# Kernel tuning notes

Hardware: AMD Instinct MI355X
Metric: run time of the kernel (lower is better)

Reference implementation:

```python
import jax, jax.numpy as jnp
import numpy as np

B = 32
NEG_INF = -1e30


def _conv2d(x, w, b):
    # x: (B,C,H,W), w: (O,I,kh,kw), VALID, stride 1
    y = jax.lax.conv_general_dilated(x, w, (1, 1), 'VALID',
                                     dimension_numbers=('NCHW', 'OIHW', 'NCHW'))
    return y + b[None, :, None, None]


def _maxpool_3_2_1(x):
    return jax.lax.reduce_window(x, NEG_INF, jax.lax.max,
                                 (1, 1, 3, 3), (1, 1, 2, 2),
                                 ((0, 0), (0, 0), (1, 1), (1, 1)))


def _extract_patches(x, kh, kw, stride):
    # x: (B,C,H,W) -> (B,C,oh,kh,ow,kw)
    H, W = x.shape[2], x.shape[3]
    oh = (H - kh) // stride + 1
    ow = (W - kw) // stride + 1
    rows = jnp.arange(oh)[:, None] * stride + jnp.arange(kh)[None, :]  # (oh,kh)
    cols = jnp.arange(ow)[:, None] * stride + jnp.arange(kw)[None, :]  # (ow,kw)
    return x[:, :, rows][:, :, :, :, cols]  # (B,C,oh,kh,ow,kw)


def _local_conv(x, w, b, stride):
    # unshared-weight conv. w: (oh,ow,oc,ic,kh,kw), b: (oc,oh,ow)
    kh, kw = w.shape[4], w.shape[5]
    p = _extract_patches(x, kh, kw, stride)              # (B,ic,oh,kh,ow,kw)
    y = jnp.einsum('bcpkql,pqockl->bopq', p, w)          # (B,oc,oh,ow)
    return y + b[None]


def setup_inputs() -> dict:
    key = jax.random.key(0)
    ks = jax.random.split(key, 14)
    s = 0.05
    f32 = jnp.float32
    inp = {
        'x': jax.random.normal(ks[0], (B, 3, 152, 152), dtype=f32),
        'conv1_w': jax.random.normal(ks[1], (32, 3, 11, 11), dtype=f32) * s,
        'conv1_b': jax.random.normal(ks[2], (32,), dtype=f32) * s,
        'conv2_w': jax.random.normal(ks[3], (16, 32, 9, 9), dtype=f32) * s,
        'conv2_b': jax.random.normal(ks[4], (16,), dtype=f32) * s,
        'lc1_w': jax.random.normal(ks[5], (55, 55, 16, 16, 9, 9), dtype=f32) * s,
        'lc1_b': jax.random.normal(ks[6], (16, 55, 55), dtype=f32) * s,
        'lc2_w': jax.random.normal(ks[7], (25, 25, 16, 16, 7, 7), dtype=f32) * s,
        'lc2_b': jax.random.normal(ks[8], (16, 25, 25), dtype=f32) * s,
        'lc3_w': jax.random.normal(ks[9], (21, 21, 16, 16, 5, 5), dtype=f32) * s,
        'lc3_b': jax.random.normal(ks[10], (16, 21, 21), dtype=f32) * s,
        'fc1_w': jax.random.normal(ks[11], (4096, 16 * 21 * 21), dtype=f32) * s,
        'fc1_b': jax.random.normal(ks[12], (4096,), dtype=f32) * s,
    }
    return inp


def reference(x, conv1_w, conv1_b, conv2_w, conv2_b,
              lc1_w, lc1_b, lc2_w, lc2_b, lc3_w, lc3_b,
              fc1_w, fc1_b):
    h = jax.nn.relu(_conv2d(x, conv1_w, conv1_b))        # (B,32,142,142)
    h = _maxpool_3_2_1(h)                                # (B,32,71,71)
    h = jax.nn.relu(_conv2d(h, conv2_w, conv2_b))        # (B,16,63,63)
    h = jax.nn.relu(_local_conv(h, lc1_w, lc1_b, 1))     # (B,16,55,55)
    h = jax.nn.relu(_local_conv(h, lc2_w, lc2_b, 2))     # (B,16,25,25)
    h = jax.nn.relu(_local_conv(h, lc3_w, lc3_b, 1))     # (B,16,21,21)
    h = h.reshape(h.shape[0], 16 * 21 * 21)
    return h @ fc1_w.T + fc1_b                           # (B,4096)
```

## Files before the change

kernel.cpp:

```cpp
#include <hip/hip_runtime.h>
#include <cstddef>

typedef __attribute__((ext_vector_type(8))) short bf16x8;
typedef __attribute__((ext_vector_type(8), aligned(8))) short bf16x8a;
typedef __attribute__((ext_vector_type(4))) float f32x4;
typedef __attribute__((ext_vector_type(4))) unsigned short u16x4;
typedef __attribute__((ext_vector_type(8))) unsigned short u16x8;

__device__ inline unsigned short f2bf(float f) {
  unsigned int u = __float_as_uint(f);
  unsigned int r = (u + 0x7FFFu + ((u >> 16) & 1u)) >> 16;
  return (unsigned short)r;
}
__device__ inline float bf2f(unsigned short u) {
  return __uint_as_float((unsigned int)u << 16);
}

__global__ __launch_bounds__(256) void prep_xb1(const float* __restrict__ x,
                                                unsigned short* __restrict__ xb) {
  const int j = blockIdx.x * 256 + threadIdx.x;
  const int iw = j % 160;
  const int ih = (j / 160) % 152;
  const int b = j / (160 * 152);
  unsigned short v[4] = {0, 0, 0, 0};
  if (iw < 152) {
    #pragma unroll
    for (int ic = 0; ic < 3; ++ic)
      v[ic] = f2bf(x[(size_t)(b * 3 + ic) * 23104 + ih * 152 + iw]);
  }
  *(unsigned long long*)(xb + ((((size_t)ih * 160 + iw) * 32) + b) * 4) =
      *(unsigned long long*)v;
}

__global__ __launch_bounds__(256) void prep_wb1(const float* __restrict__ w,
                                                unsigned short* __restrict__ wb) {
  const int j = blockIdx.x * 256 + threadIdx.x;
  const int e = j & 7;
  const int s = (j >> 3) & 31;
  const int kcj = j >> 8;
  const int kc = kcj & 3, step = kcj >> 2;
  const int t = step * 8 + kc * 2 + (e >> 2);
  const int ics = e & 3;
  const int kh = t / 12, kwp = t - kh * 12;
  float val = 0.f;
  if (t < 132 && kwp < 11 && ics < 3)
    val = w[((s * 3 + ics) * 11 + kh) * 11 + kwp];
  wb[j] = f2bf(val);
}

__global__ __launch_bounds__(256, 4) void conv1_mfma(const unsigned short* __restrict__ xb,
                                                     const unsigned short* __restrict__ wb,
                                                     const float* __restrict__ bias,
                                                     unsigned short* __restrict__ outB) {
  const int lane = threadIdx.x & 63;
  const int wvi = threadIdx.x >> 6;
  const int pos = blockIdx.x * 4 + wvi;
  const int oh = pos / 142, ow = pos % 142;
  const int row = lane & 15;
  const int kc = lane >> 4;
  f32x4 a00 = {0.f, 0.f, 0.f, 0.f}, a01 = a00, a10 = a00, a11 = a00;

  #pragma unroll 2
  for (int j = 0; j < 17; ++j) {
    const int t0 = j * 8 + 2 * kc;
    int kh = t0 / 12;
    int kwp = t0 - kh * 12;
    if (t0 >= 132) { kh = 0; kwp = 0; }
    const bf16x8 wa0 = *(const bf16x8*)(wb + (((j * 4 + kc) * 32) + row) * 8);
    const bf16x8 wa1 = *(const bf16x8*)(wb + (((j * 4 + kc) * 32) + 16 + row) * 8);
    const size_t base = (((size_t)(oh + kh) * 160) + (ow + kwp)) * 128;
    const unsigned short* xp0 = xb + base + row * 4;
    bf16x8 xv0, xv1;
    ((unsigned long long*)&xv0)[0] = *(const unsigned long long*)(xp0);
    ((unsigned long long*)&xv0)[1] = *(const unsigned long long*)(xp0 + 128);
    ((unsigned long long*)&xv1)[0] = *(const unsigned long long*)(xp0 + 64);
    ((unsigned long long*)&xv1)[1] = *(const unsigned long long*)(xp0 + 192);
    a00 = __builtin_amdgcn_mfma_f32_16x16x32_bf16(wa0, xv0, a00, 0, 0, 0);
    a01 = __builtin_amdgcn_mfma_f32_16x16x32_bf16(wa0, xv1, a01, 0, 0, 0);
    a10 = __builtin_amdgcn_mfma_f32_16x16x32_bf16(wa1, xv0, a10, 0, 0, 0);
    a11 = __builtin_amdgcn_mfma_f32_16x16x32_bf16(wa1, xv1, a11, 0, 0, 0);
  }

  unsigned short* ob = outB + (size_t)pos * 1024;
  u16x4 p00, p01, p10, p11;
  #pragma unroll
  for (int r = 0; r < 4; ++r) {
    const float bv0 = bias[kc * 4 + r];
    const float bv1 = bias[16 + kc * 4 + r];
    p00[r] = f2bf(fmaxf(a00[r] + bv0, 0.f));
    p01[r] = f2bf(fmaxf(a01[r] + bv0, 0.f));
    p10[r] = f2bf(fmaxf(a10[r] + bv1, 0.f));
    p11[r] = f2bf(fmaxf(a11[r] + bv1, 0.f));
  }
  *(u16x4*)(ob + row * 32 + kc * 4) = p00;
  *(u16x4*)(ob + (row + 16) * 32 + kc * 4) = p01;
  *(u16x4*)(ob + row * 32 + 16 + kc * 4) = p10;
  *(u16x4*)(ob + (row + 16) * 32 + 16 + kc * 4) = p11;
}

__global__ __launch_bounds__(256) void pool_t2(const unsigned short* __restrict__ in,
                                               unsigned short* __restrict__ xb) {
  const int tid = threadIdx.x;
  const int b = tid & 31, pg = tid >> 5;
  const int posp = blockIdx.x * 8 + pg;
  if (posp >= 5041) return;
  const int ohp = posp / 71, owp = posp % 71;
  u16x8 m[4];
  #pragma unroll
  for (int q = 0; q < 4; ++q)
    #pragma unroll
    for (int e = 0; e < 8; ++e) m[q][e] = 0;

  #pragma unroll
  for (int kh = 0; kh < 3; ++kh) {
    const int ih = ohp * 2 - 1 + kh;
    if (ih < 0 || ih >= 142) continue;
    #pragma unroll
    for (int kw = 0; kw < 3; ++kw) {
      const int iw = owp * 2 - 1 + kw;
      if (iw < 0 || iw >= 142) continue;
      const u16x8* p =
          (const u16x8*)(in + (((size_t)(ih * 142 + iw)) * 32 + b) * 32);
      #pragma unroll
      for (int q = 0; q < 4; ++q) {
        const u16x8 v = p[q];
        #pragma unroll
        for (int e = 0; e < 8; ++e) m[q][e] = (v[e] > m[q][e]) ? v[e] : m[q][e];
      }
    }
  }
  u16x8* o = (u16x8*)(xb + ((size_t)posp * 32 + b) * 32);
  #pragma unroll
  for (int q = 0; q < 4; ++q) o[q] = m[q];
}

__global__ __launch_bounds__(256) void prep_wb2(const float* __restrict__ w,
                                                unsigned short* __restrict__ wb) {
  const int j = blockIdx.x * 256 + threadIdx.x;
  if (j >= 81 * 16 * 32) return;
  const int ic = j & 31, oc = (j >> 5) & 15, sp = j >> 9;
  wb[j] = f2bf(w[(size_t)oc * 2592 + ic * 81 + sp]);
}

__global__ __launch_bounds__(256) void conv2_mfma(const unsigned short* __restrict__ xb,
                                                  const unsigned short* __restrict__ wb,
                                                  const float* __restrict__ bias,
                                                  unsigned short* __restrict__ outB) {
  const int lane = threadIdx.x & 63;
  const int wvi = threadIdx.x >> 6;
  int pos = blockIdx.x * 4 + wvi;
  if (pos > 3968) pos = 3968;
  const int oh = pos / 63, ow = pos % 63;
  const int row = lane & 15;
  const int kc = lane >> 4;
  f32x4 acc0 = {0.f, 0.f, 0.f, 0.f}, acc1 = {0.f, 0.f, 0.f, 0.f};
  const unsigned short* xbase = xb + (size_t)(oh * 71 + ow) * 1024;
  const int aoff = row * 32 + kc * 8;
  const int boff0 = aoff;
  const int boff1 = (row + 16) * 32 + kc * 8;

  #pragma unroll
  for (int kh = 0; kh < 9; ++kh) {
    #pragma unroll
    for (int kw = 0; kw < 9; ++kw) {
      const int sp = kh * 9 + kw;
      const bf16x8 a = *(const bf16x8*)(wb + sp * 512 + aoff);
      const unsigned short* xp = xbase + (kh * 71 + kw) * 1024;
      const bf16x8 b0 = *(const bf16x8*)(xp + boff0);
      const bf16x8 b1 = *(const bf16x8*)(xp + boff1);
      acc0 = __builtin_amdgcn_mfma_f32_16x16x32_bf16(a, b0, acc0, 0, 0, 0);
      acc1 = __builtin_amdgcn_mfma_f32_16x16x32_bf16(a, b1, acc1, 0, 0, 0);
    }
  }

  u16x4 pk0, pk1;
  #pragma unroll
  for (int r = 0; r < 4; ++r) {
    const float bv = bias[kc * 4 + r];
    pk0[r] = f2bf(fmaxf(acc0[r] + bv, 0.f));
    pk1[r] = f2bf(fmaxf(acc1[r] + bv, 0.f));
  }
  *(u16x4*)(outB + (size_t)pos * 512 + row * 16 + kc * 4) = pk0;
  *(u16x4*)(outB + (size_t)pos * 512 + (row + 16) * 16 + kc * 4) = pk1;
}

template <int KH>
__global__ __launch_bounds__(256) void prep_lcw(const float* __restrict__ w,
                                                unsigned short* __restrict__ wbT,
                                                int pos_base) {
  constexpr int KHW = KH * KH;
  constexpr int P = (KHW + 1) / 2;
  __shared__ float ls[8 * 16 * KHW];
  const int tid = threadIdx.x;
  const float* wp = w + (size_t)(pos_base + blockIdx.x) * (256 * KHW);
  unsigned short* ob = wbT + (size_t)blockIdx.x * (P * 512);

  for (int half = 0; half < 2; ++half) {
    __syncthreads();
    for (int j = tid; j < 8 * 16 * KHW; j += 256)
      ls[j] = wp[half * (8 * 16 * KHW) + j];
    __syncthreads();
    for (int j = tid; j < P * 256; j += 256) {
      const int ic = j & 15, tl = (j >> 4) & 1, oc8 = (j >> 5) & 7, pair = j >> 8;
      const int tap = pair * 2 + tl;
      const float v = (tap < KHW) ? ls[(oc8 * 16 + ic) * KHW + tap] : 0.f;
      ob[(size_t)pair * 512 + (half * 8 + oc8) * 32 + tl * 16 + ic] = f2bf(v);
    }
  }
}

template <int KH, int S, int IH, int OH>
__global__ __launch_bounds__(256) void lc_mfma(const unsigned short* __restrict__ xb,
                                               const unsigned short* __restrict__ wbT,
                                               const float* __restrict__ bias,
                                               unsigned short* __restrict__ out,
                                               int pos_base, int pos_count) {
  constexpr int KHW = KH * KH;
  constexpr int P = (KHW + 1) / 2;
  constexpr int NPOS = OH * OH;
  const int lane = threadIdx.x & 63;
  const int wvi = threadIdx.x >> 6;
  int lpos = blockIdx.x * 4 + wvi;
  if (lpos >= pos_count) lpos = pos_count - 1;
  const int pos = pos_base + lpos;
  const int oh = pos / OH, ow = pos % OH;
  const int bcol = lane & 15;
  const int kc = lane >> 4;
  const int tsel = kc >> 1;
  const int icoff = (kc & 1) * 8;
  f32x4 acc0 = {0.f, 0.f, 0.f, 0.f}, acc1 = {0.f, 0.f, 0.f, 0.f};
  const unsigned short* wp = wbT + (size_t)lpos * (P * 512) + bcol * 32 + kc * 8;
  const int xorg = (oh * S) * IH + ow * S;

  #pragma unroll
  for (int p = 0; p < P; ++p) {
    const int t0 = 2 * p;
    const int t1 = (2 * p + 1 < KHW) ? 2 * p + 1 : 2 * p;
    const int o0 = (t0 / KH) * IH + (t0 % KH);
    const int o1 = (t1 / KH) * IH + (t1 % KH);
    const int osel = tsel ? o1 : o0;
    const bf16x8 a = *(const bf16x8*)(wp + p * 512);
    const unsigned short* xp = xb + (size_t)(xorg + osel) * 512 + icoff;
    const bf16x8 b0 = *(const bf16x8*)(xp + bcol * 16);
    const bf16x8 b1 = *(const bf16x8*)(xp + (bcol + 16) * 16);
    acc0 = __builtin_amdgcn_mfma_f32_16x16x32_bf16(a, b0, acc0, 0, 0, 0);
    acc1 = __builtin_amdgcn_mfma_f32_16x16x32_bf16(a, b1, acc1, 0, 0, 0);
  }

  u16x4 pk0, pk1;
  #pragma unroll
  for (int r = 0; r < 4; ++r) {
    const float bv = bias[(kc * 4 + r) * NPOS + pos];
    pk0[r] = f2bf(fmaxf(acc0[r] + bv, 0.f));
    pk1[r] = f2bf(fmaxf(acc1[r] + bv, 0.f));
  }
  *(u16x4*)(out + (size_t)pos * 512 + bcol * 16 + kc * 4) = pk0;
  *(u16x4*)(out + (size_t)pos * 512 + (bcol + 16) * 16 + kc * 4) = pk1;
}

__global__ __launch_bounds__(256) void fc_reformat2(const unsigned short* __restrict__ xb5,
                                                    float* __restrict__ xB) {
  const int j = blockIdx.x * 256 + threadIdx.x;
  const int k = j % 7056;
  const int b = j / 7056;
  const int oc = k / 441, pos = k % 441;
  xB[j] = bf2f(xb5[((size_t)pos * 32 + b) * 16 + oc]);
}

__global__ __launch_bounds__(256) void fc1_v5(const float* __restrict__ xB,
                                              const float* __restrict__ w,
                                              float* __restrict__ part) {
  const int lane = threadIdx.x & 63;
  const int b0 = (threadIdx.x >> 6) * 8;
  const int n0 = blockIdx.x * 8;
  const int kch = blockIdx.y;
  const int kbase = kch * 1764;
  float acc[8][8] = {};
  for (int it = 0; it < 7; ++it) {
    const int ko = it * 256 + lane * 4;
    const int kb = kbase + ko;
    float4 wf[8], xr[8];
    if (ko < 1764) {
      #pragma unroll
      for (int n = 0; n < 8; ++n)
        wf[n] = *(const float4*)&w[(size_t)(n0 + n) * 7056 + kb];
      #pragma unroll
      for (int bb = 0; bb < 8; ++bb)
        xr[bb] = *(const float4*)&xB[(size_t)(b0 + bb) * 7056 + kb];
    } else {
      #pragma unroll
      for (int n = 0; n < 8; ++n) wf[n] = make_float4(0.f, 0.f, 0.f, 0.f);
      #pragma unroll
      for (int bb = 0; bb < 8; ++bb) xr[bb] = make_float4(0.f, 0.f, 0.f, 0.f);
    }
    #pragma unroll
    for (int n = 0; n < 8; ++n)
      #pragma unroll
      for (int bb = 0; bb < 8; ++bb) {
        acc[n][bb] += wf[n].x * xr[bb].x + wf[n].y * xr[bb].y +
                      wf[n].z * xr[bb].z + wf[n].w * xr[bb].w;
      }
  }
  #pragma unroll
  for (int n = 0; n < 8; ++n)
    #pragma unroll
    for (int c = 0; c < 8; ++c)
      #pragma unroll
      for (int m = 1; m < 64; m <<= 1)
        acc[n][c] += __shfl_xor(acc[n][c], m, 64);
  float val = 0.f;
  #pragma unroll
  for (int n = 0; n < 8; ++n)
    #pragma unroll
    for (int c = 0; c < 8; ++c)
      if (lane == n * 8 + c) val = acc[n][c];
  const int n_l = lane >> 3, b_l = lane & 7;
  part[(((size_t)kch * 4096 + n0 + n_l) * 32) + b0 + b_l] = val;
}

__global__ __launch_bounds__(256) void fc_combine(const float* __restrict__ part,
                                                  const float* __restrict__ bias,
                                                  float* __restrict__ out) {
  const int j = blockIdx.x * 256 + threadIdx.x;
  const int n = j & 4095, b = j >> 12;
  float v = bias[n];
  #pragma unroll
  for (int k = 0; k < 4; ++k) v += part[(((size_t)k * 4096 + n) * 32) + b];
  out[(size_t)b * 4096 + n] = v;
}

extern "C" void kernel_launch(void* const* d_in, const int* in_sizes, int n_in,
                              void* d_out, int out_size, void* d_ws, size_t ws_size,
                              hipStream_t stream) {
  const float* x       = (const float*)d_in[0];
  const float* conv1_w = (const float*)d_in[1];
  const float* conv1_b = (const float*)d_in[2];
  const float* conv2_w = (const float*)d_in[3];
  const float* conv2_b = (const float*)d_in[4];
  const float* lc1_w   = (const float*)d_in[5];
  const float* lc1_b   = (const float*)d_in[6];
  const float* lc2_w   = (const float*)d_in[7];
  const float* lc2_b   = (const float*)d_in[8];
  const float* lc3_w   = (const float*)d_in[9];
  const float* lc3_b   = (const float*)d_in[10];
  const float* fc1_w   = (const float*)d_in[11];
  const float* fc1_b   = (const float*)d_in[12];
  float* out = (float*)d_out;
  char* ws = (char*)d_ws;

  unsigned short* xb1 = (unsigned short*)(ws + 0);
  unsigned short* wb1 = (unsigned short*)(ws + 6291456);
  unsigned short* c1B = (unsigned short*)(ws + 8388608);
  unsigned short* xb2 = (unsigned short*)(ws + 50331648);
  unsigned short* wb2 = (unsigned short*)(ws + 62914560);
  unsigned short* h2b = (unsigned short*)(ws + 67108864);
  unsigned short* xb3 = (unsigned short*)(ws + 71303168);
  unsigned short* xb4 = (unsigned short*)(ws + 75497472);
  unsigned short* xb5 = (unsigned short*)(ws + 76546048);
  float* xB           = (float*)(ws + 77594624);
  float* fcp          = (float*)(ws + 78643200);
  unsigned short* wbT = (unsigned short*)(ws + 0);

  prep_xb1<<<3040, 256, 0, stream>>>(x, xb1);
  prep_wb1<<<68, 256, 0, stream>>>(conv1_w, wb1);
  conv1_mfma<<<5041, 256, 0, stream>>>(xb1, wb1, conv1_b, c1B);
  pool_t2<<<631, 256, 0, stream>>>(c1B, xb2);
  prep_wb2<<<162, 256, 0, stream>>>(conv2_w, wb2);
  conv2_mfma<<<993, 256, 0, stream>>>(xb2, wb2, conv2_b, h2b);

  prep_lcw<9><<<1513, 256, 0, stream>>>(lc1_w, wbT, 0);
  lc_mfma<9, 1, 63, 55><<<379, 256, 0, stream>>>(h2b, wbT, lc1_b, xb3, 0, 1513);
  prep_lcw<9><<<1512, 256, 0, stream>>>(lc1_w, wbT, 1513);
  lc_mfma<9, 1, 63, 55><<<378, 256, 0, stream>>>(h2b, wbT, lc1_b, xb3, 1513, 1512);

  prep_lcw<7><<<625, 256, 0, stream>>>(lc2_w, wbT, 0);
  lc_mfma<7, 2, 55, 25><<<157, 256, 0, stream>>>(xb3, wbT, lc2_b, xb4, 0, 625);

  prep_lcw<5><<<441, 256, 0, stream>>>(lc3_w, wbT, 0);
  lc_mfma<5, 1, 25, 21><<<111, 256, 0, stream>>>(xb4, wbT, lc3_b, xb5, 0, 441);

  fc_reformat2<<<882, 256, 0, stream>>>(xb5, xB);
  fc1_v5<<<dim3(512, 4), 256, 0, stream>>>(xB, fc1_w, fcp);
  fc_combine<<<512, 256, 0, stream>>>(fcp, fc1_b, out);
}
```

Before: 401.9 us.

## Merge prep kernels, prepack all local-conv weights at once, batch MFMA operand loads

Folds the input and weight prep kernels together, and the pool and conv2-weight prep together, cutting the launch count. All three local-conv weight repacks now run in one launch into separate workspace regions, so the lc1 MFMA kernel runs once instead of twice. The conv2 and local-conv MFMA loops now load four steps of operands before issuing their MFMAs, giving the scheduler more memory-level parallelism. The workspace layout grows considerably, and the larger operand batches raise register pressure.

New measurement: 379.3 us. -5.6%, faster.

```diff
diff --git a/kernel.cpp b/kernel.cpp
--- a/kernel.cpp
+++ b/kernel.cpp
@@ -16,36 +16,37 @@
   return __uint_as_float((unsigned int)u << 16);
 }
 
-__global__ __launch_bounds__(256) void prep_xb1(const float* __restrict__ x,
-                                                unsigned short* __restrict__ xb) {
-  const int j = blockIdx.x * 256 + threadIdx.x;
-  const int iw = j % 160;
-  const int ih = (j / 160) % 152;
-  const int b = j / (160 * 152);
-  unsigned short v[4] = {0, 0, 0, 0};
-  if (iw < 152) {
-    #pragma unroll
-    for (int ic = 0; ic < 3; ++ic)
-      v[ic] = f2bf(x[(size_t)(b * 3 + ic) * 23104 + ih * 152 + iw]);
-  }
-  *(unsigned long long*)(xb + ((((size_t)ih * 160 + iw) * 32) + b) * 4) =
-      *(unsigned long long*)v;
-}
-
-__global__ __launch_bounds__(256) void prep_wb1(const float* __restrict__ w,
-                                                unsigned short* __restrict__ wb) {
-  const int j = blockIdx.x * 256 + threadIdx.x;
-  const int e = j & 7;
-  const int s = (j >> 3) & 31;
-  const int kcj = j >> 8;
-  const int kc = kcj & 3, step = kcj >> 2;
-  const int t = step * 8 + kc * 2 + (e >> 2);
-  const int ics = e & 3;
-  const int kh = t / 12, kwp = t - kh * 12;
-  float val = 0.f;
-  if (t < 132 && kwp < 11 && ics < 3)
-    val = w[((s * 3 + ics) * 11 + kh) * 11 + kwp];
-  wb[j] = f2bf(val);
+__global__ __launch_bounds__(256) void prep_x1w1(const float* __restrict__ x,
+                                                 const float* __restrict__ w,
+                                                 unsigned short* __restrict__ xb,
+                                                 unsigned short* __restrict__ wb) {
+  if (blockIdx.x < 3040) {
+    const int j = blockIdx.x * 256 + threadIdx.x;
+    const int iw = j % 160;
+    const int ih = (j / 160) % 152;
+    const int b = j / (160 * 152);
+    unsigned short v[4] = {0, 0, 0, 0};
+    if (iw < 152) {
+      #pragma unroll
+      for (int ic = 0; ic < 3; ++ic)
+        v[ic] = f2bf(x[(size_t)(b * 3 + ic) * 23104 + ih * 152 + iw]);
+    }
+    *(unsigned long long*)(xb + ((((size_t)ih * 160 + iw) * 32) + b) * 4) =
+        *(unsigned long long*)v;
+  } else {
+    const int j = (blockIdx.x - 3040) * 256 + threadIdx.x;
+    const int e = j & 7;
+    const int s = (j >> 3) & 31;
+    const int kcj = j >> 8;
+    const int kc = kcj & 3, step = kcj >> 2;
+    const int t = step * 8 + kc * 2 + (e >> 2);
+    const int ics = e & 3;
+    const int kh = t / 12, kwp = t - kh * 12;
+    float val = 0.f;
+    if (t < 132 && kwp < 11 && ics < 3)
+      val = w[((s * 3 + ics) * 11 + kh) * 11 + kwp];
+    wb[j] = f2bf(val);
+  }
 }
 
 __global__ __launch_bounds__(256, 4) void conv1_mfma(const unsigned short* __restrict__ xb,
@@ -98,48 +99,48 @@
   *(u16x4*)(ob + (row + 16) * 32 + 16 + kc * 4) = p11;
 }
 
-__global__ __launch_bounds__(256) void pool_t2(const unsigned short* __restrict__ in,
-                                               unsigned short* __restrict__ xb) {
-  const int tid = threadIdx.x;
-  const int b = tid & 31, pg = tid >> 5;
-  const int posp = blockIdx.x * 8 + pg;
-  if (posp >= 5041) return;
-  const int ohp = posp / 71, owp = posp % 71;
-  u16x8 m[4];
-  #pragma unroll
-  for (int q = 0; q < 4; ++q)
-    #pragma unroll
-    for (int e = 0; e < 8; ++e) m[q][e] = 0;
-
-  #pragma unroll
-  for (int kh = 0; kh < 3; ++kh) {
-    const int ih = ohp * 2 - 1 + kh;
-    if (ih < 0 || ih >= 142) continue;
-    #pragma unroll
-    for (int kw = 0; kw < 3; ++kw) {
-      const int iw = owp * 2 - 1 + kw;
-      if (iw < 0 || iw >= 142) continue;
-      const u16x8* p =
-          (const u16x8*)(in + (((size_t)(ih * 142 + iw)) * 32 + b) * 32);
-      #pragma unroll
-      for (int q = 0; q < 4; ++q) {
-        const u16x8 v = p[q];
+__global__ __launch_bounds__(256) void poolt2_wb2(const unsigned short* __restrict__ in,
+                                                  unsigned short* __restrict__ xb,
+                                                  const float* __restrict__ w2,
+                                                  unsigned short* __restrict__ wb2) {
+  if (blockIdx.x < 631) {
+    const int tid = threadIdx.x;
+    const int b = tid & 31, pg = tid >> 5;
+    const int posp = blockIdx.x * 8 + pg;
+    if (posp >= 5041) return;
+    const int ohp = posp / 71, owp = posp % 71;
+    u16x8 m[4];
+    #pragma unroll
+    for (int q = 0; q < 4; ++q)
+      #pragma unroll
+      for (int e = 0; e < 8; ++e) m[q][e] = 0;
+
+    #pragma unroll
+    for (int kh = 0; kh < 3; ++kh) {
+      const int ih = ohp * 2 - 1 + kh;
+      if (ih < 0 || ih >= 142) continue;
+      #pragma unroll
+      for (int kw = 0; kw < 3; ++kw) {
+        const int iw = owp * 2 - 1 + kw;
+        if (iw < 0 || iw >= 142) continue;
+        const u16x8* p =
+            (const u16x8*)(in + (((size_t)(ih * 142 + iw)) * 32 + b) * 32);
         #pragma unroll
-        for (int e = 0; e < 8; ++e) m[q][e] = (v[e] > m[q][e]) ? v[e] : m[q][e];
+        for (int q = 0; q < 4; ++q) {
+          const u16x8 v = p[q];
+          #pragma unroll
+          for (int e = 0; e < 8; ++e) m[q][e] = (v[e] > m[q][e]) ? v[e] : m[q][e];
+        }
       }
     }
-  }
-  u16x8* o = (u16x8*)(xb + ((size_t)posp * 32 + b) * 32);
-  #pragma unroll
-  for (int q = 0; q < 4; ++q) o[q] = m[q];
-}
-
-__global__ __launch_bounds__(256) void prep_wb2(const float* __restrict__ w,
-                                                unsigned short* __restrict__ wb) {
-  const int j = blockIdx.x * 256 + threadIdx.x;
-  if (j >= 81 * 16 * 32) return;
-  const int ic = j & 31, oc = (j >> 5) & 15, sp = j >> 9;
-  wb[j] = f2bf(w[(size_t)oc * 2592 + ic * 81 + sp]);
+    u16x8* o = (u16x8*)(xb + ((size_t)posp * 32 + b) * 32);
+    #pragma unroll
+    for (int q = 0; q < 4; ++q) o[q] = m[q];
+  } else {
+    const int j = (blockIdx.x - 631) * 256 + threadIdx.x;
+    const int ic = j & 31, oc = (j >> 5) & 15, sp = j >> 9;
+    wb2[j] = f2bf(w2[(size_t)oc * 2592 + ic * 81 + sp]);
+  }
 }
 
 __global__ __launch_bounds__(256) void conv2_mfma(const unsigned short* __restrict__ xb,
@@ -160,17 +161,30 @@
   const int boff1 = (row + 16) * 32 + kc * 8;
 
   #pragma unroll
-  for (int kh = 0; kh < 9; ++kh) {
-    #pragma unroll
-    for (int kw = 0; kw < 9; ++kw) {
-      const int sp = kh * 9 + kw;
-      const bf16x8 a = *(const bf16x8*)(wb + sp * 512 + aoff);
+  for (int g = 0; g < 20; ++g) {
+    bf16x8 A[4], Ba[4], Bb[4];
+    #pragma unroll
+    for (int i = 0; i < 4; ++i) {
+      const int sp = g * 4 + i;
+      const int kh = sp / 9, kw = sp - kh * 9;
+      A[i] = *(const bf16x8*)(wb + sp * 512 + aoff);
       const unsigned short* xp = xbase + (kh * 71 + kw) * 1024;
-      const bf16x8 b0 = *(const bf16x8*)(xp + boff0);
-      const bf16x8 b1 = *(const bf16x8*)(xp + boff1);
-      acc0 = __builtin_amdgcn_mfma_f32_16x16x32_bf16(a, b0, acc0, 0, 0, 0);
-      acc1 = __builtin_amdgcn_mfma_f32_16x16x32_bf16(a, b1, acc1, 0, 0, 0);
-    }
+      Ba[i] = *(const bf16x8*)(xp + boff0);
+      Bb[i] = *(const bf16x8*)(xp + boff1);
+    }
+    #pragma unroll
+    for (int i = 0; i < 4; ++i) {
+      acc0 = __builtin_amdgcn_mfma_f32_16x16x32_bf16(A[i], Ba[i], acc0, 0, 0, 0);
+      acc1 = __builtin_amdgcn_mfma_f32_16x16x32_bf16(A[i], Bb[i], acc1, 0, 0, 0);
+    }
+  }
+  {
+    const bf16x8 a = *(const bf16x8*)(wb + 80 * 512 + aoff);
+    const unsigned short* xp = xbase + (8 * 71 + 8) * 1024;
+    const bf16x8 b0 = *(const bf16x8*)(xp + boff0);
+    const bf16x8 b1 = *(const bf16x8*)(xp + boff1);
+    acc0 = __builtin_amdgcn_mfma_f32_16x16x32_bf16(a, b0, acc0, 0, 0, 0);
+    acc1 = __builtin_amdgcn_mfma_f32_16x16x32_bf16(a, b1, acc1, 0, 0, 0);
   }
 
   u16x4 pk0, pk1;
@@ -184,16 +198,28 @@
   *(u16x4*)(outB + (size_t)pos * 512 + (row + 16) * 16 + kc * 4) = pk1;
 }
 
-template <int KH>
-__global__ __launch_bounds__(256) void prep_lcw(const float* __restrict__ w,
-                                                unsigned short* __restrict__ wbT,
-                                                int pos_base) {
-  constexpr int KHW = KH * KH;
-  constexpr int P = (KHW + 1) / 2;
-  __shared__ float ls[8 * 16 * KHW];
+__global__ __launch_bounds__(256) void prep_lcw_all(const float* __restrict__ w1,
+                                                    unsigned short* __restrict__ o1,
+                                                    const float* __restrict__ w2,
+                                                    unsigned short* __restrict__ o2,
+                                                    const float* __restrict__ w3,
+                                                    unsigned short* __restrict__ o3) {
+  __shared__ float ls[8 * 16 * 81];
+  int blk = blockIdx.x;
+  const float* wp;
+  unsigned short* ob;
+  int KHW;
+  if (blk < 3025) {
+    KHW = 81; wp = w1 + (size_t)blk * 256 * 81; ob = o1 + (size_t)blk * 41 * 512;
+  } else if (blk < 3650) {
+    blk -= 3025;
+    KHW = 49; wp = w2 + (size_t)blk * 256 * 49; ob = o2 + (size_t)blk * 25 * 512;
+  } else {
+    blk -= 3650;
+    KHW = 25; wp = w3 + (size_t)blk * 256 * 25; ob = o3 + (size_t)blk * 13 * 512;
+  }
+  const int P = (KHW + 1) / 2;
   const int tid = threadIdx.x;
-  const float* wp = w + (size_t)(pos_base + blockIdx.x) * (256 * KHW);
-  unsigned short* ob = wbT + (size_t)blockIdx.x * (P * 512);
 
   for (int half = 0; half < 2; ++half) {
     __syncthreads();
@@ -214,7 +240,7 @@
                                                const unsigned short* __restrict__ wbT,
                                                const float* __restrict__ bias,
                                                unsigned short* __restrict__ out,
-                                               int pos_base, int pos_count) {
+                                               int pos_count) {
   constexpr int KHW = KH * KH;
   constexpr int P = (KHW + 1) / 2;
   constexpr int NPOS = OH * OH;
@@ -222,7 +248,7 @@
   const int wvi = threadIdx.x >> 6;
   int lpos = blockIdx.x * 4 + wvi;
   if (lpos >= pos_count) lpos = pos_count - 1;
-  const int pos = pos_base + lpos;
+  const int pos = lpos;
   const int oh = pos / OH, ow = pos % OH;
   const int bcol = lane & 15;
   const int kc = lane >> 4;
@@ -233,14 +259,32 @@
   const int xorg = (oh * S) * IH + ow * S;
 
   #pragma unroll
-  for (int p = 0; p < P; ++p) {
+  for (int g = 0; g < P / 4; ++g) {
+    bf16x8 A[4], Ba[4], Bb[4];
+    #pragma unroll
+    for (int i = 0; i < 4; ++i) {
+      const int p = g * 4 + i;
+      const int t0 = 2 * p, t1 = 2 * p + 1;
+      const int o0 = (t0 / KH) * IH + (t0 % KH);
+      const int o1 = (t1 / KH) * IH + (t1 % KH);
+      const int osel = tsel ? o1 : o0;
+      A[i] = *(const bf16x8*)(wp + p * 512);
+      const unsigned short* xp = xb + (size_t)(xorg + osel) * 512 + icoff;
+      Ba[i] = *(const bf16x8*)(xp + bcol * 16);
+      Bb[i] = *(const bf16x8*)(xp + (bcol + 16) * 16);
+    }
+    #pragma unroll
+    for (int i = 0; i < 4; ++i) {
+      acc0 = __builtin_amdgcn_mfma_f32_16x16x32_bf16(A[i], Ba[i], acc0, 0, 0, 0);
+      acc1 = __builtin_amdgcn_mfma_f32_16x16x32_bf16(A[i], Bb[i], acc1, 0, 0, 0);
+    }
+  }
+  {
+    constexpr int p = P - 1;
     const int t0 = 2 * p;
-    const int t1 = (2 * p + 1 < KHW) ? 2 * p + 1 : 2 * p;
     const int o0 = (t0 / KH) * IH + (t0 % KH);
-    const int o1 = (t1 / KH) * IH + (t1 % KH);
-    const int osel = tsel ? o1 : o0;
     const bf16x8 a = *(const bf16x8*)(wp + p * 512);
-    const unsigned short* xp = xb + (size_t)(xorg + osel) * 512 + icoff;
+    const unsigned short* xp = xb + (size_t)(xorg + o0) * 512 + icoff;
     const bf16x8 b0 = *(const bf16x8*)(xp + bcol * 16);
     const bf16x8 b1 = *(const bf16x8*)(xp + (bcol + 16) * 16);
     acc0 = __builtin_amdgcn_mfma_f32_16x16x32_bf16(a, b0, acc0, 0, 0, 0);
@@ -348,36 +392,30 @@
   float* out = (float*)d_out;
   char* ws = (char*)d_ws;
 
-  unsigned short* xb1 = (unsigned short*)(ws + 0);
-  unsigned short* wb1 = (unsigned short*)(ws + 6291456);
-  unsigned short* c1B = (unsigned short*)(ws + 8388608);
-  unsigned short* xb2 = (unsigned short*)(ws + 50331648);
-  unsigned short* wb2 = (unsigned short*)(ws + 62914560);
-  unsigned short* h2b = (unsigned short*)(ws + 67108864);
-  unsigned short* xb3 = (unsigned short*)(ws + 71303168);
-  unsigned short* xb4 = (unsigned short*)(ws + 75497472);
-  unsigned short* xb5 = (unsigned short*)(ws + 76546048);
-  float* xB           = (float*)(ws + 77594624);
-  float* fcp          = (float*)(ws + 78643200);
-  unsigned short* wbT = (unsigned short*)(ws + 0);
-
-  prep_xb1<<<3040, 256, 0, stream>>>(x, xb1);
-  prep_wb1<<<68, 256, 0, stream>>>(conv1_w, wb1);
+  unsigned short* xb1  = (unsigned short*)(ws + 0);
+  unsigned short* wb1  = (unsigned short*)(ws + 8388608);
+  unsigned short* c1B  = (unsigned short*)(ws + 16777216);
+  unsigned short* xb2  = (unsigned short*)(ws + 67108864);
+  unsigned short* wb2  = (unsigned short*)(ws + 83886080);
+  unsigned short* h2b  = (unsigned short*)(ws + 92274688);
+  unsigned short* xb3  = (unsigned short*)(ws + 100663296);
+  unsigned short* xb4  = (unsigned short*)(ws + 109051904);
+  unsigned short* xb5  = (unsigned short*)(ws + 117440512);
+  float* xB            = (float*)(ws + 125829120);
+  float* fcp           = (float*)(ws + 134217728);
+  unsigned short* wbT1 = (unsigned short*)(ws + 167772160);
+  unsigned short* wbT2 = (unsigned short*)(ws + 301989888);
+  unsigned short* wbT3 = (unsigned short*)(ws + 318767104);
+
+  prep_x1w1<<<3108, 256, 0, stream>>>(x, conv1_w, xb1, wb1);
   conv1_mfma<<<5041, 256, 0, stream>>>(xb1, wb1, conv1_b, c1B);
-  pool_t2<<<631, 256, 0, stream>>>(c1B, xb2);
-  prep_wb2<<<162, 256, 0, stream>>>(conv2_w, wb2);
+  poolt2_wb2<<<793, 256, 0, stream>>>(c1B, xb2, conv2_w, wb2);
   conv2_mfma<<<993, 256, 0, stream>>>(xb2, wb2, conv2_b, h2b);
 
-  prep_lcw<9><<<1513, 256, 0, stream>>>(lc1_w, wbT, 0);
-  lc_mfma<9, 1, 63, 55><<<379, 256, 0, stream>>>(h2b, wbT, lc1_b, xb3, 0, 1513);
-  prep_lcw<9><<<1512, 256, 0, stream>>>(lc1_w, wbT, 1513);
-  lc_mfma<9, 1, 63, 55><<<378, 256, 0, stream>>>(h2b, wbT, lc1_b, xb3, 1513, 1512);
-
-  prep_lcw<7><<<625, 256, 0, stream>>>(lc2_w, wbT, 0);
-  lc_mfma<7, 2, 55, 25><<<157, 256, 0, stream>>>(xb3, wbT, lc2_b, xb4, 0, 625);
-
-  prep_lcw<5><<<441, 256, 0, stream>>>(lc3_w, wbT, 0);
-  lc_mfma<5, 1, 25, 21><<<111, 256, 0, stream>>>(xb4, wbT, lc3_b, xb5, 0, 441);
+  prep_lcw_all<<<4091, 256, 0, stream>>>(lc1_w, wbT1, lc2_w, wbT2, lc3_w, wbT3);
+  lc_mfma<9, 1, 63, 55><<<757, 256, 0, stream>>>(h2b, wbT1, lc1_b, xb3, 3025);
+  lc_mfma<7, 2, 55, 25><<<157, 256, 0, stream>>>(xb3, wbT2, lc2_b, xb4, 625);
+  lc_mfma<5, 1, 25, 21><<<111, 256, 0, stream>>>(xb4, wbT3, lc3_b, xb5, 441);
 
   fc_reformat2<<<882, 256, 0, stream>>>(xb5, xB);
   fc1_v5<<<dim3(512, 4), 256, 0, stream>>>(xB, fc1_w, fcp);
```
